# Kernel tuning notes

Hardware: AMD Instinct MI355X
Metric: run time of the kernel (lower is better)

Reference implementation:

```python
import jax, jax.numpy as jnp
import numpy as np

N_HEAD = 16
D = 1024
LV = 2048
HEAD_DIM = D // N_HEAD
B = 2
LQ = 2048
LN_EPS = 1e-5


def setup_inputs() -> dict:
    key = jax.random.key(0)
    ks = jax.random.split(key, 8)
    s = 0.02
    v = jax.random.normal(ks[0], (B, LV, D), dtype=jnp.float32)
    q = jax.random.normal(ks[1], (B, LQ, D), dtype=jnp.float32)
    # per-head attn linear: d -> lv
    Wa = jax.random.normal(ks[2], (N_HEAD, D, LV), dtype=jnp.float32) * s
    ba = jnp.zeros((N_HEAD, LV), dtype=jnp.float32)
    # per-head layernorm over d
    gamma = jnp.ones((N_HEAD, D), dtype=jnp.float32)
    beta = jnp.zeros((N_HEAD, D), dtype=jnp.float32)
    # per-head proj (FilteredLinear modeled as affine): d -> head_dim
    Wp = jax.random.normal(ks[3], (N_HEAD, D, HEAD_DIM), dtype=jnp.float32) * s
    bp = jnp.zeros((N_HEAD, HEAD_DIM), dtype=jnp.float32)
    return {"v": v, "q": q, "Wa": Wa, "ba": ba, "gamma": gamma,
            "beta": beta, "Wp": Wp, "bp": bp}


def _mha(v, q, Wa, ba, gamma, beta, Wp, bp):
    # attn: [H, B, Lq, Lv] = relu(q @ Wa_h + ba_h)  (batched across heads)
    attn = jax.nn.relu(jnp.einsum('bqd,hdl->hbql', q, Wa)
                       + ba[:, None, None, :])
    # external-attention aggregation: [H, B, Lq, D]
    agg = jnp.einsum('hbql,bld->hbqd', attn, v)
    # per-head LayerNorm over last dim (d)
    mu = jnp.mean(agg, axis=-1, keepdims=True)
    var = jnp.var(agg, axis=-1, keepdims=True)
    normed = (agg - mu) * jax.lax.rsqrt(var + LN_EPS)
    normed = normed * gamma[:, None, None, :] + beta[:, None, None, :]
    # per-head projection to head_dim: [H, B, Lq, head_dim]
    heads = jnp.einsum('hbqd,hde->hbqe', normed, Wp) + bp[:, None, None, :]
    # concat heads along feature dim -> [B, Lq, D]
    return heads.transpose(1, 2, 0, 3).reshape(q.shape[0], q.shape[1], -1)


def reference(v, q, Wa, ba, gamma, beta, Wp, bp):
    return _mha(v, q, Wa, ba, gamma, beta, Wp, bp)
```

## Files before the change

### kernel.cpp

```cpp
#include <hip/hip_runtime.h>
#include <hip/hip_bf16.h>

typedef __attribute__((ext_vector_type(8))) short short8;
typedef __attribute__((ext_vector_type(4))) float f32x4;

#define N_HEAD 16
#define DMODEL 1024
#define LV 2048
#define LQ 2048
#define BATCH 2
#define HEAD_DIM 64

template <int N> struct IC { static constexpr int v = N; };

__device__ inline ushort f2bf(float f) {
    union { float f; unsigned u; } v; v.f = f;
    unsigned r = v.u + 0x7fffu + ((v.u >> 16) & 1u);
    return (ushort)(r >> 16);
}
__device__ inline float bf2f(ushort h) {
    union { unsigned u; float f; } v; v.u = ((unsigned)h) << 16;
    return v.f;
}

__global__ __launch_bounds__(256) void cast_bf16(const float* __restrict__ src,
                                                 ushort* __restrict__ dst, int n) {
    int i = (blockIdx.x * 256 + threadIdx.x) * 4;
    if (i < n) {
        float4 v = *(const float4*)(src + i);
        ushort4 o;
        o.x = f2bf(v.x); o.y = f2bf(v.y); o.z = f2bf(v.z); o.w = f2bf(v.w);
        *(ushort4*)(dst + i) = o;
    }
}

__global__ __launch_bounds__(256) void transpose_cast(const float* __restrict__ src,
                                                      ushort* __restrict__ dst,
                                                      int R, int C) {
    __shared__ float t[32][33];
    size_t zoff = (size_t)blockIdx.z * R * C;
    int c0 = blockIdx.x * 32, r0 = blockIdx.y * 32;
    int tx = threadIdx.x, ty = threadIdx.y;
#pragma unroll
    for (int i = 0; i < 4; ++i)
        t[ty + i * 8][tx] = src[zoff + (size_t)(r0 + ty + i * 8) * C + c0 + tx];
    __syncthreads();
#pragma unroll
    for (int i = 0; i < 4; ++i)
        dst[zoff + (size_t)(c0 + ty + i * 8) * R + r0 + tx] = f2bf(t[tx][ty + i * 8]);
}

template <bool RELU>
__global__ __launch_bounds__(512, 2) void gemm256(
    const ushort* __restrict__ A, const ushort* __restrict__ B,
    ushort* __restrict__ Cout, const float* __restrict__ bias,
    int K,
    long sA_b, long sA_h, long sB_b, long sB_h, long sC_z, int ldc, long sBias_h)
{
    __shared__ __align__(16) char smem[131072];

    const int z = blockIdx.z, b = z & 1, h = z >> 1;
    A += (size_t)b * sA_b + (size_t)h * sA_h;
    B += (size_t)b * sB_b + (size_t)h * sB_h;
    const float* biasp = bias ? bias + (size_t)h * sBias_h : nullptr;

    const int bm0 = blockIdx.y * 256;
    const int bn0 = blockIdx.x * 256;
    const int T = threadIdx.x;
    const int lane = T & 63, wid = T >> 6;
    const int wr = wid >> 2, wc = wid & 3;
    const int fr = lane & 15, fq = lane >> 4;
    const int laneoff = fr * 64 + ((fq * 16) ^ ((fr >> 3) << 5));

    const char* pA0 = smem + 0     + wr * 8192 + laneoff;
    const char* pB0 = smem + 32768 + wc * 4096 + laneoff;
    const char* pA1 = pA0 + 65536;
    const char* pB1 = pB0 + 65536;

    const int s_row = T >> 2;
    const int s_csw = ((T & 3) * 16) ^ (((T >> 5) & 1) << 5);
    const ushort* gA = A + (size_t)(bm0 + s_row) * K + (s_csw >> 1);
    const ushort* gB = B + (size_t)(bn0 + s_row) * K + (s_csw >> 1);

    const int nt = K >> 6;

    auto stage = [&](int op, int kh, int db, int snext) {
        const ushort* g = op ? gB : gA;
        const size_t kbase = (size_t)snext * 64 + kh * 32;
        char* d = smem + db * 65536 + op * 32768 + kh * 16384 + (T << 4);
#pragma unroll
        for (int j = 0; j < 2; ++j) {
            __builtin_amdgcn_global_load_lds(
                (const __attribute__((address_space(1))) void*)(g + (size_t)j * 128 * K + kbase),
                (__attribute__((address_space(3))) void*)(d + j * 8192), 16, 0, 0);
        }
    };

    f32x4 acc[8][4];
#pragma unroll
    for (int m = 0; m < 8; ++m)
#pragma unroll
        for (int n = 0; n < 4; ++n)
#pragma unroll
            for (int j = 0; j < 4; ++j) acc[m][n][j] = 0.f;

    auto phase = [&](const char* pA, const char* pB, short8* bfr, int s, int db,
                     auto MH, auto KH, auto RDB, auto DOST, auto SOP, auto SKH, auto VM) {
        constexpr int mh = decltype(MH)::v, kh = decltype(KH)::v;
        short8 a[4];
#pragma unroll
        for (int i = 0; i < 4; ++i)
            a[i] = *(const short8*)(pA + kh * 16384 + (mh * 4 + i) * 1024);
        if constexpr (decltype(RDB)::v) {
#pragma unroll
            for (int n = 0; n < 4; ++n)
                bfr[n] = *(const short8*)(pB + kh * 16384 + n * 1024);
        }
        if constexpr (decltype(DOST)::v)
            stage(decltype(SOP)::v, decltype(SKH)::v, db ^ 1, s + 1);
        asm volatile("s_barrier" ::: "memory");
        asm volatile("s_waitcnt lgkmcnt(0)" ::: "memory");
        __builtin_amdgcn_sched_barrier(0);
        __builtin_amdgcn_s_setprio(1);
#pragma unroll
        for (int i = 0; i < 4; ++i)
#pragma unroll
            for (int n = 0; n < 4; ++n)
                acc[mh * 4 + i][n] = __builtin_amdgcn_mfma_f32_16x16x32_bf16(
                    a[i], bfr[n], acc[mh * 4 + i][n], 0, 0, 0);
        __builtin_amdgcn_s_setprio(0);
        __builtin_amdgcn_sched_barrier(0);
        constexpr int vm = decltype(VM)::v;
        if constexpr (vm == 4) asm volatile("s_waitcnt vmcnt(4)" ::: "memory");
        else if constexpr (vm == 0) asm volatile("s_waitcnt vmcnt(0)" ::: "memory");
        asm volatile("s_barrier" ::: "memory");
    };

    auto step_full = [&](int s, const char* pA, const char* pB, int db) {
        short8 bfr[4];
        phase(pA, pB, bfr, s, db, IC<0>{}, IC<0>{}, IC<1>{}, IC<1>{}, IC<0>{}, IC<0>{}, IC<-1>{});
        phase(pA, pB, bfr, s, db, IC<1>{}, IC<0>{}, IC<0>{}, IC<1>{}, IC<1>{}, IC<0>{}, IC<4>{});
        phase(pA, pB, bfr, s, db, IC<0>{}, IC<1>{}, IC<1>{}, IC<1>{}, IC<0>{}, IC<1>{}, IC<-1>{});
        phase(pA, pB, bfr, s, db, IC<1>{}, IC<1>{}, IC<0>{}, IC<1>{}, IC<1>{}, IC<1>{}, IC<4>{});
    };
    auto step_last = [&](int s, const char* pA, const char* pB, int db) {
        short8 bfr[4];
        phase(pA, pB, bfr, s, db, IC<0>{}, IC<0>{}, IC<1>{}, IC<0>{}, IC<0>{}, IC<0>{}, IC<-1>{});
        phase(pA, pB, bfr, s, db, IC<1>{}, IC<0>{}, IC<0>{}, IC<0>{}, IC<0>{}, IC<0>{}, IC<0>{});
        phase(pA, pB, bfr, s, db, IC<0>{}, IC<1>{}, IC<1>{}, IC<0>{}, IC<0>{}, IC<0>{}, IC<-1>{});
        phase(pA, pB, bfr, s, db, IC<1>{}, IC<1>{}, IC<0>{}, IC<0>{}, IC<0>{}, IC<0>{}, IC<-1>{});
    };

    stage(0, 0, 0, 0); stage(1, 0, 0, 0); stage(0, 1, 0, 0); stage(1, 1, 0, 0);
    asm volatile("s_waitcnt vmcnt(4)" ::: "memory");
    asm volatile("s_barrier" ::: "memory");

    for (int s = 0; s < nt - 2; s += 2) {
        step_full(s,     pA0, pB0, 0);
        step_full(s + 1, pA1, pB1, 1);
    }
    step_full(nt - 2, pA0, pB0, 0);
    step_last(nt - 1, pA1, pB1, 1);

    ushort* C = Cout + (size_t)z * sC_z;
    const int row0 = bm0 + wr * 128;
    const int col0 = bn0 + wc * 64;
#pragma unroll
    for (int n = 0; n < 4; ++n) {
        const int c = col0 + n * 16 + fr;
        const float bvv = biasp ? biasp[c] : 0.f;
#pragma unroll
        for (int m = 0; m < 8; ++m) {
            const int r = row0 + m * 16 + fq * 4;
#pragma unroll
            for (int j = 0; j < 4; ++j) {
                float val = acc[m][n][j] + bvv;
                if (RELU) val = fmaxf(val, 0.f);
                C[(size_t)(r + j) * ldc + c] = f2bf(val);
            }
        }
    }
}

__global__ __launch_bounds__(256) void ln_kernel(ushort* __restrict__ agg,
                                                 const float* __restrict__ gamma,
                                                 const float* __restrict__ beta) {
    const int wid = threadIdx.x >> 6, lane = threadIdx.x & 63;
    const size_t row = (size_t)blockIdx.x * 4 + wid;
    const int h = (int)(row >> 12);
    ushort* p = agg + row * 1024 + lane * 16;
    short8 r0 = *(const short8*)p;
    short8 r1 = *(const short8*)(p + 8);
    float x[16];
#pragma unroll
    for (int j = 0; j < 8; ++j) { x[j] = bf2f((ushort)r0[j]); x[8 + j] = bf2f((ushort)r1[j]); }
    float s = 0.f, s2 = 0.f;
#pragma unroll
    for (int j = 0; j < 16; ++j) { s += x[j]; s2 += x[j] * x[j]; }
    for (int o = 1; o < 64; o <<= 1) {
        s  += __shfl_xor(s,  o, 64);
        s2 += __shfl_xor(s2, o, 64);
    }
    float mu  = s * (1.0f / 1024.0f);
    float var = s2 * (1.0f / 1024.0f) - mu * mu;
    float rs  = rsqrtf(fmaxf(var, 0.f) + 1e-5f);
    const float* g  = gamma + (size_t)h * 1024 + lane * 16;
    const float* bt = beta  + (size_t)h * 1024 + lane * 16;
    short8 o0, o1;
#pragma unroll
    for (int j = 0; j < 8; ++j) {
        o0[j] = (short)f2bf((x[j]     - mu) * rs * g[j]     + bt[j]);
        o1[j] = (short)f2bf((x[8 + j] - mu) * rs * g[8 + j] + bt[8 + j]);
    }
    *(short8*)p = o0;
    *(short8*)(p + 8) = o1;
}

__global__ __launch_bounds__(256) void proj_kernel(const ushort* __restrict__ normed,
                                                   const ushort* __restrict__ WpT,
                                                   const float* __restrict__ bp,
                                                   float* __restrict__ out,
                                                   int h_base) {
    const int z = blockIdx.y, b = z & 1, h = z >> 1;
    const int hg = h_base + h;
    const int wid = threadIdx.x >> 6, lane = threadIdx.x & 63;
    const int fr = lane & 15, fq = lane >> 4;
    const int m0 = (blockIdx.x * 4 + wid) * 16;

    const ushort* Abase = normed + ((size_t)z * 2048 + m0 + fr) * 1024 + fq * 8;
    const ushort* Bbase = WpT + (size_t)hg * 64 * 1024 + (size_t)fr * 1024 + fq * 8;

    f32x4 acc[4];
#pragma unroll
    for (int n = 0; n < 4; ++n)
#pragma unroll
        for (int j = 0; j < 4; ++j) acc[n][j] = 0.f;

    for (int kt = 0; kt < 32; ++kt) {
        short8 a = *(const short8*)(Abase + kt * 32);
#pragma unroll
        for (int n = 0; n < 4; ++n) {
            short8 bb = *(const short8*)(Bbase + n * 16 * 1024 + kt * 32);
            acc[n] = __builtin_amdgcn_mfma_f32_16x16x32_bf16(a, bb, acc[n], 0, 0, 0);
        }
    }
#pragma unroll
    for (int n = 0; n < 4; ++n) {
        int c = hg * 64 + n * 16 + fr;
        float bvv = bp[hg * 64 + n * 16 + fr];
#pragma unroll
        for (int j = 0; j < 4; ++j)
            out[(size_t)b * 2048 * 1024 + (size_t)(m0 + fq * 4 + j) * 1024 + c] =
                acc[n][j] + bvv;
    }
}

extern "C" void kernel_launch(void* const* d_in, const int* in_sizes, int n_in,
                              void* d_out, int out_size, void* d_ws, size_t ws_size,
                              hipStream_t stream) {
    const float* v     = (const float*)d_in[0];
    const float* q     = (const float*)d_in[1];
    const float* Wa    = (const float*)d_in[2];
    const float* ba    = (const float*)d_in[3];
    const float* gamma = (const float*)d_in[4];
    const float* beta  = (const float*)d_in[5];
    const float* Wp    = (const float*)d_in[6];
    const float* bp    = (const float*)d_in[7];
    float* out = (float*)d_out;

    const size_t MB = 1ull << 20;
    char* ws = (char*)d_ws;
    ushort* qbf = (ushort*)(ws);
    ushort* vT  = (ushort*)(ws + 8 * MB);
    ushort* WpT = (ushort*)(ws + 16 * MB);
    int NH = 1;
    {
        const int cands[5] = {16, 8, 4, 2, 1};
        for (int i = 0; i < 5; ++i) {
            if ((size_t)(18 + 28 * cands[i]) * MB <= ws_size) { NH = cands[i]; break; }
        }
    }
    ushort* WaT_c  = (ushort*)(ws + 18 * MB);
    ushort* attn_c = (ushort*)(ws + (18 + (size_t)4 * NH) * MB);
    ushort* agg_c  = (ushort*)(ws + (18 + (size_t)20 * NH) * MB);

    dim3 tb(32, 8);
    cast_bf16<<<4096, 256, 0, stream>>>(q, qbf, BATCH * LQ * DMODEL);
    transpose_cast<<<dim3(DMODEL / 32, LV / 32, BATCH), tb, 0, stream>>>(v, vT, LV, DMODEL);
    transpose_cast<<<dim3(HEAD_DIM / 32, DMODEL / 32, N_HEAD), tb, 0, stream>>>(Wp, WpT, DMODEL, HEAD_DIM);

    for (int h0 = 0; h0 < N_HEAD; h0 += NH) {
        transpose_cast<<<dim3(LV / 32, DMODEL / 32, NH), tb, 0, stream>>>(
            Wa + (size_t)h0 * DMODEL * LV, WaT_c, DMODEL, LV);

        gemm256<true><<<dim3(LV / 256, LQ / 256, NH * 2), 512, 0, stream>>>(
            qbf, WaT_c, attn_c, ba + (size_t)h0 * LV, DMODEL,
            (long)LQ * DMODEL, 0L,
            0L, (long)LV * DMODEL,
            (long)LQ * LV, LV, (long)LV);

        gemm256<false><<<dim3(DMODEL / 256, LQ / 256, NH * 2), 512, 0, stream>>>(
            attn_c, vT, agg_c, nullptr, LV,
            (long)LQ * LV, (long)2 * LQ * LV,
            (long)DMODEL * LV, 0L,
            (long)LQ * DMODEL, DMODEL, 0L);

        ln_kernel<<<(NH * 2 * LQ) / 4, 256, 0, stream>>>(
            agg_c, gamma + (size_t)h0 * DMODEL, beta + (size_t)h0 * DMODEL);

        proj_kernel<<<dim3(LQ / 64, NH * 2), 256, 0, stream>>>(
            agg_c, WpT, bp, out, h0);
    }
}
```

Before: 817.0 us.

## Fuse LayerNorm into projection, remap GEMM blocks per XCD, stage epilogue via LDS

The GEMM grid is flattened to 1D and block ids are remapped so consecutive tiles of the same head and batch land on the same XCD (gid&7 chunking), which should improve L2 reuse. The GEMM epilogue now writes bf16 results into shared memory and stores them to global memory as 16-byte row-contiguous vectors instead of scattered 2-byte stores. The separate LayerNorm kernel is removed: the projection kernel first computes row statistics from the agg buffer, then normalizes on the fly before the MFMAs. This saves one full read-write pass over agg, at the cost of reading agg twice inside the projection kernel.

```diff
diff --git a/kernel.cpp b/kernel.cpp
--- a/kernel.cpp
+++ b/kernel.cpp
@@ -50,7 +50,7 @@
         dst[zoff + (size_t)(c0 + ty + i * 8) * R + r0 + tx] = f2bf(t[tx][ty + i * 8]);
 }
 
-template <bool RELU>
+template <bool RELU, int LNA, int ZSH, bool BMFAST>
 __global__ __launch_bounds__(512, 2) void gemm256(
     const ushort* __restrict__ A, const ushort* __restrict__ B,
     ushort* __restrict__ Cout, const float* __restrict__ bias,
@@ -59,13 +59,20 @@
 {
     __shared__ __align__(16) char smem[131072];
 
-    const int z = blockIdx.z, b = z & 1, h = z >> 1;
+    const int gid = blockIdx.x;
+    const int per = (int)gridDim.x >> 3;
+    const int w = (gid & 7) * per + (gid >> 3);
+    const int z = w >> ZSH;
+    const int rem = w & ((1 << ZSH) - 1);
+    int bm0, bn0;
+    if (BMFAST) { bm0 = (rem & ((1 << LNA) - 1)) * 256; bn0 = (rem >> LNA) * 256; }
+    else        { bn0 = (rem & ((1 << LNA) - 1)) * 256; bm0 = (rem >> LNA) * 256; }
+
+    const int b = z & 1, h = z >> 1;
     A += (size_t)b * sA_b + (size_t)h * sA_h;
     B += (size_t)b * sB_b + (size_t)h * sB_h;
     const float* biasp = bias ? bias + (size_t)h * sBias_h : nullptr;
 
-    const int bm0 = blockIdx.y * 256;
-    const int bn0 = blockIdx.x * 256;
     const int T = threadIdx.x;
     const int lane = T & 63, wid = T >> 6;
     const int wr = wid >> 2, wc = wid & 3;
@@ -162,73 +169,69 @@
     step_full(nt - 2, pA0, pB0, 0);
     step_last(nt - 1, pA1, pB1, 1);
 
+    asm volatile("s_waitcnt vmcnt(0) lgkmcnt(0)" ::: "memory");
+    __builtin_amdgcn_s_barrier();
     ushort* C = Cout + (size_t)z * sC_z;
-    const int row0 = bm0 + wr * 128;
     const int col0 = bn0 + wc * 64;
-#pragma unroll
-    for (int n = 0; n < 4; ++n) {
-        const int c = col0 + n * 16 + fr;
-        const float bvv = biasp ? biasp[c] : 0.f;
-#pragma unroll
-        for (int m = 0; m < 8; ++m) {
-            const int r = row0 + m * 16 + fq * 4;
-#pragma unroll
-            for (int j = 0; j < 4; ++j) {
-                float val = acc[m][n][j] + bvv;
-                if (RELU) val = fmaxf(val, 0.f);
-                C[(size_t)(r + j) * ldc + c] = f2bf(val);
+    const int rl = lane >> 3, cb = lane & 7;
+#pragma unroll
+    for (int r = 0; r < 2; ++r) {
+        if (wr == r) {
+            char* eb = smem + wc * 18432;
+#pragma unroll
+            for (int n = 0; n < 4; ++n) {
+                const float bvv = biasp ? biasp[col0 + n * 16 + fr] : 0.f;
+#pragma unroll
+                for (int m = 0; m < 8; ++m) {
+#pragma unroll
+                    for (int j = 0; j < 4; ++j) {
+                        float val = acc[m][n][j] + bvv;
+                        if (RELU) val = fmaxf(val, 0.f);
+                        *(ushort*)(eb + (m * 16 + fq * 4 + j) * 144 + (n * 16 + fr) * 2) = f2bf(val);
+                    }
+                }
             }
-        }
-    }
-}
-
-__global__ __launch_bounds__(256) void ln_kernel(ushort* __restrict__ agg,
-                                                 const float* __restrict__ gamma,
-                                                 const float* __restrict__ beta) {
-    const int wid = threadIdx.x >> 6, lane = threadIdx.x & 63;
-    const size_t row = (size_t)blockIdx.x * 4 + wid;
-    const int h = (int)(row >> 12);
-    ushort* p = agg + row * 1024 + lane * 16;
-    short8 r0 = *(const short8*)p;
-    short8 r1 = *(const short8*)(p + 8);
-    float x[16];
-#pragma unroll
-    for (int j = 0; j < 8; ++j) { x[j] = bf2f((ushort)r0[j]); x[8 + j] = bf2f((ushort)r1[j]); }
-    float s = 0.f, s2 = 0.f;
-#pragma unroll
-    for (int j = 0; j < 16; ++j) { s += x[j]; s2 += x[j] * x[j]; }
-    for (int o = 1; o < 64; o <<= 1) {
-        s  += __shfl_xor(s,  o, 64);
-        s2 += __shfl_xor(s2, o, 64);
-    }
-    float mu  = s * (1.0f / 1024.0f);
-    float var = s2 * (1.0f / 1024.0f) - mu * mu;
-    float rs  = rsqrtf(fmaxf(var, 0.f) + 1e-5f);
-    const float* g  = gamma + (size_t)h * 1024 + lane * 16;
-    const float* bt = beta  + (size_t)h * 1024 + lane * 16;
-    short8 o0, o1;
-#pragma unroll
-    for (int j = 0; j < 8; ++j) {
-        o0[j] = (short)f2bf((x[j]     - mu) * rs * g[j]     + bt[j]);
-        o1[j] = (short)f2bf((x[8 + j] - mu) * rs * g[8 + j] + bt[8 + j]);
-    }
-    *(short8*)p = o0;
-    *(short8*)(p + 8) = o1;
-}
-
-__global__ __launch_bounds__(256) void proj_kernel(const ushort* __restrict__ normed,
-                                                   const ushort* __restrict__ WpT,
-                                                   const float* __restrict__ bp,
-                                                   float* __restrict__ out,
-                                                   int h_base) {
-    const int z = blockIdx.y, b = z & 1, h = z >> 1;
-    const int hg = h_base + h;
+            asm volatile("s_waitcnt lgkmcnt(0)" ::: "memory");
+            const int row0 = bm0 + r * 128;
+#pragma unroll
+            for (int i = 0; i < 16; ++i) {
+                short8 vv = *(const short8*)(eb + (i * 8 + rl) * 144 + cb * 16);
+                *(short8*)(C + (size_t)(row0 + i * 8 + rl) * ldc + col0 + cb * 8) = vv;
+            }
+        }
+        __builtin_amdgcn_s_barrier();
+    }
+}
+
+__global__ __launch_bounds__(256) void lnproj_kernel(const ushort* __restrict__ agg,
+                                                     const ushort* __restrict__ WpT,
+                                                     const float* __restrict__ gamma,
+                                                     const float* __restrict__ beta,
+                                                     const float* __restrict__ bp,
+                                                     float* __restrict__ out,
+                                                     int h_base) {
+    const int z = blockIdx.y, b = z & 1, hg = h_base + (z >> 1);
     const int wid = threadIdx.x >> 6, lane = threadIdx.x & 63;
     const int fr = lane & 15, fq = lane >> 4;
     const int m0 = (blockIdx.x * 4 + wid) * 16;
 
-    const ushort* Abase = normed + ((size_t)z * 2048 + m0 + fr) * 1024 + fq * 8;
+    const ushort* Arow = agg + ((size_t)z * 2048 + m0 + fr) * 1024 + fq * 8;
+
+    float s = 0.f, s2 = 0.f;
+    for (int kt = 0; kt < 32; ++kt) {
+        short8 a = *(const short8*)(Arow + kt * 32);
+#pragma unroll
+        for (int j = 0; j < 8; ++j) { float x = bf2f((ushort)a[j]); s += x; s2 += x * x; }
+    }
+    s  += __shfl_xor(s, 16, 64);  s2 += __shfl_xor(s2, 16, 64);
+    s  += __shfl_xor(s, 32, 64);  s2 += __shfl_xor(s2, 32, 64);
+    const float mu  = s * (1.0f / 1024.0f);
+    const float var = s2 * (1.0f / 1024.0f) - mu * mu;
+    const float rs  = rsqrtf(fmaxf(var, 0.f) + 1e-5f);
+
     const ushort* Bbase = WpT + (size_t)hg * 64 * 1024 + (size_t)fr * 1024 + fq * 8;
+    const float* gp = gamma + (size_t)hg * 1024 + fq * 8;
+    const float* bt = beta  + (size_t)hg * 1024 + fq * 8;
 
     f32x4 acc[4];
 #pragma unroll
@@ -237,17 +240,29 @@
         for (int j = 0; j < 4; ++j) acc[n][j] = 0.f;
 
     for (int kt = 0; kt < 32; ++kt) {
-        short8 a = *(const short8*)(Abase + kt * 32);
+        short8 a = *(const short8*)(Arow + kt * 32);
+        float4 g0 = *(const float4*)(gp + kt * 32);
+        float4 g1 = *(const float4*)(gp + kt * 32 + 4);
+        float4 b0 = *(const float4*)(bt + kt * 32);
+        float4 b1 = *(const float4*)(bt + kt * 32 + 4);
+        const float gg[8] = {g0.x, g0.y, g0.z, g0.w, g1.x, g1.y, g1.z, g1.w};
+        const float bb_[8] = {b0.x, b0.y, b0.z, b0.w, b1.x, b1.y, b1.z, b1.w};
+        short8 an;
+#pragma unroll
+        for (int j = 0; j < 8; ++j) {
+            float xn = (bf2f((ushort)a[j]) - mu) * rs * gg[j] + bb_[j];
+            an[j] = (short)f2bf(xn);
+        }
 #pragma unroll
         for (int n = 0; n < 4; ++n) {
-            short8 bb = *(const short8*)(Bbase + n * 16 * 1024 + kt * 32);
-            acc[n] = __builtin_amdgcn_mfma_f32_16x16x32_bf16(a, bb, acc[n], 0, 0, 0);
+            short8 wv = *(const short8*)(Bbase + n * 16 * 1024 + kt * 32);
+            acc[n] = __builtin_amdgcn_mfma_f32_16x16x32_bf16(an, wv, acc[n], 0, 0, 0);
         }
     }
 #pragma unroll
     for (int n = 0; n < 4; ++n) {
-        int c = hg * 64 + n * 16 + fr;
-        float bvv = bp[hg * 64 + n * 16 + fr];
+        const int c = hg * 64 + n * 16 + fr;
+        const float bvv = bp[c];
 #pragma unroll
         for (int j = 0; j < 4; ++j)
             out[(size_t)b * 2048 * 1024 + (size_t)(m0 + fq * 4 + j) * 1024 + c] =
@@ -293,22 +308,19 @@
         transpose_cast<<<dim3(LV / 32, DMODEL / 32, NH), tb, 0, stream>>>(
             Wa + (size_t)h0 * DMODEL * LV, WaT_c, DMODEL, LV);
 
-        gemm256<true><<<dim3(LV / 256, LQ / 256, NH * 2), 512, 0, stream>>>(
+        gemm256<true, 3, 6, true><<<64 * NH * 2, 512, 0, stream>>>(
             qbf, WaT_c, attn_c, ba + (size_t)h0 * LV, DMODEL,
             (long)LQ * DMODEL, 0L,
             0L, (long)LV * DMODEL,
             (long)LQ * LV, LV, (long)LV);
 
-        gemm256<false><<<dim3(DMODEL / 256, LQ / 256, NH * 2), 512, 0, stream>>>(
+        gemm256<false, 2, 5, false><<<32 * NH * 2, 512, 0, stream>>>(
             attn_c, vT, agg_c, nullptr, LV,
             (long)LQ * LV, (long)2 * LQ * LV,
             (long)DMODEL * LV, 0L,
             (long)LQ * DMODEL, DMODEL, 0L);
 
-        ln_kernel<<<(NH * 2 * LQ) / 4, 256, 0, stream>>>(
-            agg_c, gamma + (size_t)h0 * DMODEL, beta + (size_t)h0 * DMODEL);
-
-        proj_kernel<<<dim3(LQ / 64, NH * 2), 256, 0, stream>>>(
-            agg_c, WpT, bp, out, h0);
-    }
-}
+        lnproj_kernel<<<dim3(LQ / 64, NH * 2), 256, 0, stream>>>(
+            agg_c, WpT, gamma, beta, bp, out, h0);
+    }
+}
```

Result: faster. 714.5 us (median of 3 runs) (-12.6%).
